# Optimization experiments

Measured on AMD Instinct MI355X. Metric: run time of the kernel, lower is better.

The kernel has to match this reference:

```python
import jax, jax.numpy as jnp
import numpy as np

H = 512
A = 16
L = 3
B = 256
T = 512


def layer_norm(x, g, b, eps=1e-5):
    mu = jnp.mean(x, axis=-1, keepdims=True)
    var = jnp.mean((x - mu) ** 2, axis=-1, keepdims=True)
    return (x - mu) * jax.lax.rsqrt(var + eps) * g + b


def setup_inputs() -> dict:
    key = jax.random.key(0)
    ks = jax.random.split(key, 16)
    s = 1.0 / np.sqrt(H)  # keep linear outputs O(1), mimicking orthogonal init scale
    return {
        "hidden": jnp.zeros((B, H), jnp.float32),
        "obs": jax.random.normal(ks[0], (B, T, H), jnp.float32),
        "dones": jax.random.bernoulli(ks[1], 0.01, (B, T)),
        "avail_actions": jnp.ones((B, T, A), jnp.float32),
        "in_w": jax.random.normal(ks[2], (L, H, H), jnp.float32) * s,
        "in_b": jnp.zeros((L, H), jnp.float32),
        "ln_g": jnp.ones((L, H), jnp.float32),
        "ln_b": jnp.zeros((L, H), jnp.float32),
        "gru_wih": jax.random.normal(ks[3], (3 * H, H), jnp.float32) * s,
        "gru_whh": jax.random.normal(ks[4], (3 * H, H), jnp.float32) * s,
        "gru_bih": jnp.zeros((3 * H,), jnp.float32),
        "gru_bhh": jnp.zeros((3 * H,), jnp.float32),
        "am1_w": jax.random.normal(ks[5], (H, H), jnp.float32) * s,
        "am1_b": jnp.zeros((H,), jnp.float32),
        "amln_g": jnp.ones((H,), jnp.float32),
        "amln_b": jnp.zeros((H,), jnp.float32),
        "am2_w": jax.random.normal(ks[6], (A, H), jnp.float32) * s * 0.01,
        "am2_b": jnp.zeros((A,), jnp.float32),
    }


def reference(hidden, obs, dones, avail_actions, in_w, in_b, ln_g, ln_b,
              gru_wih, gru_whh, gru_bih, gru_bhh,
              am1_w, am1_b, amln_g, amln_b, am2_w, am2_b):
    # --- pre-RNN MLP: Linear -> LayerNorm -> ReLU, x3 ---
    emb = obs  # [B,T,H]
    for l in range(L):
        emb = jax.nn.relu(layer_norm(emb @ in_w[l].T + in_b[l], ln_g[l], ln_b[l]))

    # --- GRU scan with reset masking (torch GRUCell math) ---
    def step(h, xt):
        x, r = xt  # x: [B,H], r: [B] bool
        h = jnp.where(r[:, None], 0.0, h)
        gi = x @ gru_wih.T + gru_bih  # [B,3H]
        gh = h @ gru_whh.T + gru_bhh
        i_r, i_z, i_n = jnp.split(gi, 3, axis=-1)
        h_r, h_z, h_n = jnp.split(gh, 3, axis=-1)
        rg = jax.nn.sigmoid(i_r + h_r)
        z = jax.nn.sigmoid(i_z + h_z)
        n = jnp.tanh(i_n + rg * h_n)
        h_new = (1.0 - z) * n + z * h
        return h_new, h_new

    h_final, outs = jax.lax.scan(
        step, hidden, (jnp.swapaxes(emb, 0, 1), dones.T))  # outs: [T,B,H]
    outs = jnp.swapaxes(outs, 0, 1)  # [B,T,H]

    # --- actor head ---
    am = jax.nn.relu(layer_norm(outs @ am1_w.T + am1_b, amln_g, amln_b))
    logits = am @ am2_w.T + am2_b  # [B,T,A]
    logits = logits - (1.0 - avail_actions) * 1e10
    return (h_final, logits)
```

## Files before the change

kernel.cpp:

```cpp
#include <hip/hip_runtime.h>

#define HD 512
#define AD 16
#define BD 256
#define TD 512

using short8  = __attribute__((ext_vector_type(8))) short;
using float4v = __attribute__((ext_vector_type(4))) float;
using ushort4v = __attribute__((ext_vector_type(4))) unsigned short;
typedef unsigned short u16;
typedef unsigned long long u64;

__device__ __forceinline__ u16 f2bf(float f) {
  union { float f; unsigned u; } v; v.f = f;
  unsigned r = v.u + 0x7fffu + ((v.u >> 16) & 1u);
  return (u16)(r >> 16);
}
__device__ __forceinline__ float bf2f(u16 u) {
  union { unsigned u; float f; } c; c.u = ((unsigned)u) << 16; return c.f;
}

__global__ __launch_bounds__(256) void cvt_bf16(const float* __restrict__ in,
                                                u16* __restrict__ out, int n) {
  int i = blockIdx.x * 256 + threadIdx.x;
  int stride = gridDim.x * 256;
  for (; i < n; i += stride) out[i] = f2bf(in[i]);
}

template <bool AF32>
__global__ __launch_bounds__(256) void gemm_ln_relu(
    const void* __restrict__ Ap, const u16* __restrict__ W,
    const float* __restrict__ bias, const float* __restrict__ gam,
    const float* __restrict__ bet, u16* __restrict__ Y) {
  const int r0 = blockIdx.x * 64;
  const int tid = threadIdx.x;
  const int wave = tid >> 6, lane = tid & 63;
  const int lq = lane >> 4, ln16 = lane & 15;

  __shared__ u16 As[64 * 40];
  __shared__ u16 Bs[512 * 40];
  __shared__ float partial[64][4][2];
  __shared__ float murs[64][2];

  float4v acc[4][8];
#pragma unroll
  for (int i = 0; i < 4; ++i)
#pragma unroll
    for (int j = 0; j < 8; ++j) acc[i][j] = (float4v){0.f, 0.f, 0.f, 0.f};

  for (int kk = 0; kk < 16; ++kk) {
    __syncthreads();
    if (AF32) {
      const float* Af = (const float*)Ap;
#pragma unroll
      for (int it = 0; it < 2; ++it) {
        int q = tid + it * 256;
        int row = q >> 3, ko = (q & 7) * 4;
        float4v v = *(const float4v*)(Af + (r0 + row) * 512 + kk * 32 + ko);
        ushort4v o;
        o[0] = f2bf(v[0]); o[1] = f2bf(v[1]); o[2] = f2bf(v[2]); o[3] = f2bf(v[3]);
        *(ushort4v*)(&As[row * 40 + ko]) = o;
      }
    } else {
      const u16* Ab = (const u16*)Ap;
      int row = tid >> 2, ko = (tid & 3) * 8;
      *(short8*)(&As[row * 40 + ko]) =
          *(const short8*)(Ab + (r0 + row) * 512 + kk * 32 + ko);
    }
#pragma unroll
    for (int it = 0; it < 8; ++it) {
      int q = tid + it * 256;
      int row = q >> 2, ko = (q & 3) * 8;
      *(short8*)(&Bs[row * 40 + ko]) =
          *(const short8*)(W + row * 512 + kk * 32 + ko);
    }
    __syncthreads();
    short8 afr[4];
#pragma unroll
    for (int mt = 0; mt < 4; ++mt)
      afr[mt] = *(const short8*)(&As[(mt * 16 + ln16) * 40 + lq * 8]);
#pragma unroll
    for (int nt = 0; nt < 8; ++nt) {
      short8 bfr = *(const short8*)(&Bs[(wave * 128 + nt * 16 + ln16) * 40 + lq * 8]);
#pragma unroll
      for (int mt = 0; mt < 4; ++mt)
        acc[mt][nt] = __builtin_amdgcn_mfma_f32_16x16x32_bf16(afr[mt], bfr, acc[mt][nt], 0, 0, 0);
    }
  }

  float gv[8], bv[8], av[8];
#pragma unroll
  for (int nt = 0; nt < 8; ++nt) {
    int c = wave * 128 + nt * 16 + ln16;
    gv[nt] = gam[c]; bv[nt] = bet[c]; av[nt] = bias[c];
  }
#pragma unroll
  for (int mt = 0; mt < 4; ++mt)
#pragma unroll
    for (int nt = 0; nt < 8; ++nt)
#pragma unroll
      for (int r = 0; r < 4; ++r) acc[mt][nt][r] += av[nt];

#pragma unroll
  for (int mt = 0; mt < 4; ++mt) {
#pragma unroll
    for (int r = 0; r < 4; ++r) {
      float s = 0.f, ss = 0.f;
#pragma unroll
      for (int nt = 0; nt < 8; ++nt) { float v = acc[mt][nt][r]; s += v; ss += v * v; }
#pragma unroll
      for (int off = 1; off < 16; off <<= 1) { s += __shfl_xor(s, off); ss += __shfl_xor(ss, off); }
      if (ln16 == 0) {
        int m = mt * 16 + lq * 4 + r;
        partial[m][wave][0] = s; partial[m][wave][1] = ss;
      }
    }
  }
  __syncthreads();
  if (tid < 64) {
    float s = partial[tid][0][0] + partial[tid][1][0] + partial[tid][2][0] + partial[tid][3][0];
    float ss = partial[tid][0][1] + partial[tid][1][1] + partial[tid][2][1] + partial[tid][3][1];
    float mu = s * (1.f / 512.f);
    float var = ss * (1.f / 512.f) - mu * mu;
    murs[tid][0] = mu;
    murs[tid][1] = rsqrtf(var + 1e-5f);
  }
  __syncthreads();
#pragma unroll
  for (int mt = 0; mt < 4; ++mt) {
#pragma unroll
    for (int r = 0; r < 4; ++r) {
      int m = mt * 16 + lq * 4 + r;
      float mu = murs[m][0], rs = murs[m][1];
#pragma unroll
      for (int nt = 0; nt < 8; ++nt) {
        int c = wave * 128 + nt * 16 + ln16;
        float v = (acc[mt][nt][r] - mu) * rs * gv[nt] + bv[nt];
        Y[(r0 + m) * 512 + c] = f2bf(fmaxf(v, 0.f));
      }
    }
  }
}

__global__ __launch_bounds__(256) void gru_scan(
    const u16* __restrict__ emb, const u16* __restrict__ wih,
    const u16* __restrict__ whh, const float* __restrict__ bih,
    const float* __restrict__ bhh, const float* __restrict__ hidden,
    const int* __restrict__ dones, float* __restrict__ outs,
    float* __restrict__ hfin, u64* __restrict__ hpk, int* __restrict__ cnt) {
  const int bg = blockIdx.x >> 5;
  const int cg = blockIdx.x & 31;
  const int c0 = cg * 16;
  const int b0 = bg * 32;
  const int tid = threadIdx.x;
  const int wave = tid >> 6, lane = tid & 63;
  const int lq = lane >> 4, ln16 = lane & 15;

  __shared__ u16 Wh[48 * 512];
  __shared__ float scr[2][2][3][16][18];

  for (int q = tid; q < 48 * 64; q += 256) {
    int rr = q >> 6, c = q & 63;
    int gate = rr >> 4, chl = rr & 15;
    int phys = c ^ (rr & 7);
    *(short8*)(&Wh[rr * 512 + phys * 8]) =
        *(const short8*)(whh + (gate * 512 + c0 + chl) * 512 + c * 8);
  }

  auto produce = [&](int tp, int mt) {
    int row = b0 + mt * 16 + ln16;
    const u16* ap = emb + (row * 512 + tp) * 512 + lq * 8;
    float4v acc[3];
#pragma unroll
    for (int g = 0; g < 3; ++g) acc[g] = (float4v){0.f, 0.f, 0.f, 0.f};
#pragma unroll
    for (int kk = 0; kk < 16; ++kk) {
      short8 af = *(const short8*)(ap + kk * 32);
#pragma unroll
      for (int g = 0; g < 3; ++g) {
        short8 bf = *(const short8*)(wih + (g * 512 + c0 + ln16) * 512 + lq * 8 + kk * 32);
        acc[g] = __builtin_amdgcn_mfma_f32_16x16x32_bf16(af, bf, acc[g], 0, 0, 0);
      }
    }
#pragma unroll
    for (int g = 0; g < 3; ++g)
#pragma unroll
      for (int r = 0; r < 4; ++r)
        scr[tp & 1][mt][g][lq * 4 + r][ln16] = acc[g][r];
  };

  if (wave >= 2) produce(0, wave - 2);
  __syncthreads();

  if (wave < 2) {
    const int mt = wave;
    const int rowA = b0 + mt * 16 + ln16;
    float bi[3], bhv[3];
#pragma unroll
    for (int g = 0; g < 3; ++g) {
      bi[g]  = bih[g * 512 + c0 + ln16];
      bhv[g] = bhh[g * 512 + c0 + ln16];
    }
    float hprev[4];
#pragma unroll
    for (int r = 0; r < 4; ++r)
      hprev[r] = hidden[(b0 + mt * 16 + lq * 4 + r) * 512 + c0 + ln16];

    int* mycnt = cnt + (bg * 2 + mt) * 512;

    for (int t = 0; t < TD; ++t) {
      bool dn = dones[rowA * 512 + t] != 0;
      int dn_i = dn ? 1 : 0;
      float giv[3][4];
#pragma unroll
      for (int g = 0; g < 3; ++g)
#pragma unroll
        for (int r = 0; r < 4; ++r) giv[g][r] = scr[t & 1][mt][g][lq * 4 + r][ln16];

      if (t > 0) {
        const int* cp = mycnt + (t - 1);
        int guard = 0;
        while (__hip_atomic_load(cp, __ATOMIC_RELAXED, __HIP_MEMORY_SCOPE_AGENT) < 32) {
          if (++guard > (1 << 18)) break;
        }
      }

      u64 av[32];
      if (t == 0) {
#pragma unroll
        for (int kk = 0; kk < 16; ++kk) {
          const float* hp = hidden + rowA * 512 + lq * 8 + kk * 32;
          float4v h0 = *(const float4v*)(hp);
          float4v h1 = *(const float4v*)(hp + 4);
          av[2 * kk] = (u64)f2bf(h0[0]) | ((u64)f2bf(h0[1]) << 16) |
                       ((u64)f2bf(h0[2]) << 32) | ((u64)f2bf(h0[3]) << 48);
          av[2 * kk + 1] = (u64)f2bf(h1[0]) | ((u64)f2bf(h1[1]) << 16) |
                           ((u64)f2bf(h1[2]) << 32) | ((u64)f2bf(h1[3]) << 48);
        }
      } else {
        const u64* hb = hpk + ((t - 1) & 1) * 32768 + rowA * 128 + lq * 2;
#pragma unroll
        for (int kk = 0; kk < 16; ++kk) {
          av[2 * kk]     = __hip_atomic_load(hb + kk * 8,     __ATOMIC_RELAXED, __HIP_MEMORY_SCOPE_AGENT);
          av[2 * kk + 1] = __hip_atomic_load(hb + kk * 8 + 1, __ATOMIC_RELAXED, __HIP_MEMORY_SCOPE_AGENT);
        }
      }
#pragma unroll
      for (int i = 0; i < 32; ++i) av[i] = dn ? 0ull : av[i];

      float4v agh[3];
#pragma unroll
      for (int g = 0; g < 3; ++g) agh[g] = (float4v){0.f, 0.f, 0.f, 0.f};
#pragma unroll
      for (int kk = 0; kk < 16; ++kk) {
        union { u64 q[2]; short8 v; } u;
        u.q[0] = av[2 * kk]; u.q[1] = av[2 * kk + 1];
#pragma unroll
        for (int g = 0; g < 3; ++g) {
          int rr = g * 16 + ln16;
          int phys = (lq + 4 * kk) ^ (rr & 7);
          short8 bf = *(const short8*)(&Wh[rr * 512 + phys * 8]);
          agh[g] = __builtin_amdgcn_mfma_f32_16x16x32_bf16(u.v, bf, agh[g], 0, 0, 0);
        }
      }

      float hv[4];
#pragma unroll
      for (int r = 0; r < 4; ++r) {
        int dnc = __shfl(dn_i, lq * 4 + r);
        float h = dnc ? 0.f : hprev[r];
        float ir  = giv[0][r] + bi[0];
        float iz  = giv[1][r] + bi[1];
        float inn = giv[2][r] + bi[2];
        float hr  = agh[0][r] + bhv[0];
        float hz  = agh[1][r] + bhv[1];
        float hn  = agh[2][r] + bhv[2];
        float rg = 1.f / (1.f + expf(-(ir + hr)));
        float z  = 1.f / (1.f + expf(-(iz + hz)));
        float nn = tanhf(inn + rg * hn);
        hv[r] = (1.f - z) * nn + z * h;
        hprev[r] = hv[r];
      }

#pragma unroll
      for (int r = 0; r < 4; ++r) {
        unsigned mybf = f2bf(hv[r]);
        unsigned o1 = (unsigned)__shfl((int)mybf, lane ^ 1);
        unsigned pk = (mybf & 0xffffu) | (o1 << 16);
        unsigned pk2 = (unsigned)__shfl((int)pk, lane ^ 2);
        int b = b0 + mt * 16 + lq * 4 + r;
        if ((ln16 & 3) == 0) {
          u64 pv = (u64)pk | ((u64)pk2 << 32);
          __hip_atomic_store(hpk + (t & 1) * 32768 + b * 128 + ((c0 + ln16) >> 2), pv,
                             __ATOMIC_RELAXED, __HIP_MEMORY_SCOPE_AGENT);
        }
        outs[(t * 256 + b) * 512 + c0 + ln16] = hv[r];
        if (t == TD - 1) hfin[b * 512 + c0 + ln16] = hv[r];
      }
      __builtin_amdgcn_s_waitcnt(0);
      if (lane == 0 && t < TD - 1)
        __hip_atomic_fetch_add(mycnt + t, 1, __ATOMIC_RELAXED, __HIP_MEMORY_SCOPE_AGENT);

      __syncthreads();
    }
  } else {
    const int mt = wave - 2;
    for (int t = 0; t < TD; ++t) {
      if (t + 1 < TD) produce(t + 1, mt);
      __syncthreads();
    }
  }
}

__global__ __launch_bounds__(256) void head_logits(
    const u16* __restrict__ am, const float* __restrict__ w2,
    const float* __restrict__ b2, const float* __restrict__ avail,
    float* __restrict__ out) {
  int r = blockIdx.x * 16 + (threadIdx.x >> 4);
  int a = threadIdx.x & 15;
  int t = r >> 8, b = r & 255;
  const u16* ar = am + r * 512;
  const float* wr = w2 + a * 512;
  float acc = 0.f;
  for (int k = 0; k < 512; k += 8) {
    short8 v = *(const short8*)(ar + k);
    float4v w0 = *(const float4v*)(wr + k);
    float4v w1 = *(const float4v*)(wr + k + 4);
    acc += bf2f((u16)v[0]) * w0[0] + bf2f((u16)v[1]) * w0[1] +
           bf2f((u16)v[2]) * w0[2] + bf2f((u16)v[3]) * w0[3] +
           bf2f((u16)v[4]) * w1[0] + bf2f((u16)v[5]) * w1[1] +
           bf2f((u16)v[6]) * w1[2] + bf2f((u16)v[7]) * w1[3];
  }
  int oi = (b * 512 + t) * 16 + a;
  float avv = avail[oi];
  out[oi] = acc + b2[a] - (1.f - avv) * 1e10f;
}

extern "C" void kernel_launch(void* const* d_in, const int* in_sizes, int n_in,
                              void* d_out, int out_size, void* d_ws, size_t ws_size,
                              hipStream_t stream) {
  (void)in_sizes; (void)n_in; (void)out_size; (void)ws_size;
  const float* hidden = (const float*)d_in[0];
  const float* obs    = (const float*)d_in[1];
  const int*   dones  = (const int*)d_in[2];
  const float* avail  = (const float*)d_in[3];
  const float* in_w   = (const float*)d_in[4];
  const float* in_b   = (const float*)d_in[5];
  const float* ln_g   = (const float*)d_in[6];
  const float* ln_b   = (const float*)d_in[7];
  const float* gwih   = (const float*)d_in[8];
  const float* gwhh   = (const float*)d_in[9];
  const float* gbih   = (const float*)d_in[10];
  const float* gbhh   = (const float*)d_in[11];
  const float* am1w   = (const float*)d_in[12];
  const float* am1b   = (const float*)d_in[13];
  const float* amg    = (const float*)d_in[14];
  const float* amb    = (const float*)d_in[15];
  const float* am2w   = (const float*)d_in[16];
  const float* am2b   = (const float*)d_in[17];

  char* ws = (char*)d_ws;
  u16*   embA  = (u16*)(ws);
  u16*   embB  = (u16*)(ws + 134217728);
  float* outs  = (float*)(ws + 268435456);
  u16*   w_in  = (u16*)(ws + 536870912);
  u16*   w_ih  = w_in + 786432;
  u16*   w_hh  = w_ih + 786432;
  u16*   w_a1  = w_hh + 786432;
  int*   cnt   = (int*)(ws + 536870912 + 5242880);
  u64*   hpk   = (u64*)(ws + 536870912 + 5242880 + 32768);

  hipMemsetAsync(cnt, 0, 32768, stream);
  cvt_bf16<<<1024, 256, 0, stream>>>(in_w, w_in, 786432);
  cvt_bf16<<<1024, 256, 0, stream>>>(gwih, w_ih, 786432);
  cvt_bf16<<<1024, 256, 0, stream>>>(gwhh, w_hh, 786432);
  cvt_bf16<<<512, 256, 0, stream>>>(am1w, w_a1, 262144);

  gemm_ln_relu<true ><<<2048, 256, 0, stream>>>(obs,  w_in,          in_b,        ln_g,        ln_b,        embA);
  gemm_ln_relu<false><<<2048, 256, 0, stream>>>(embA, w_in + 262144, in_b + 512,  ln_g + 512,  ln_b + 512,  embB);
  gemm_ln_relu<false><<<2048, 256, 0, stream>>>(embB, w_in + 524288, in_b + 1024, ln_g + 1024, ln_b + 1024, embA);

  gru_scan<<<256, 256, 0, stream>>>(embA, w_ih, w_hh, gbih, gbhh, hidden, dones,
                                    outs, (float*)d_out, hpk, cnt);

  gemm_ln_relu<true ><<<2048, 256, 0, stream>>>(outs, w_a1, am1b, amg, amb, embB);
  head_logits<<<8192, 256, 0, stream>>>(embB, am2w, am2b, avail, (float*)d_out + 131072);
}
```

Baseline: 4.751 ms.

## Keep GRU weights in registers, use fast sigmoid/tanh, and signal before output stores

The recurrent W_hh slice and the input W_ih slice now live in per-lane registers (48 short8 each) instead of LDS or repeated global reads, with launch bounds set to one block per CU. Gate activations use exp2/rcp hardware intrinsics instead of expf/tanhf. Done-masking now zeroes the h·W_hh products per row instead of masking the packed inputs. Each lane stores its bf16 h value directly rather than shuffle-packing into 64-bit words, and the readiness counter is bumped before the fp32 output stores so dependent blocks can start sooner. The intent is to shorten the serial per-step critical path, at the cost of very high register pressure, possible spills, and slightly less accurate transcendentals.

```diff
diff --git a/kernel.cpp b/kernel.cpp
--- a/kernel.cpp
+++ b/kernel.cpp
@@ -18,6 +18,13 @@
 }
 __device__ __forceinline__ float bf2f(u16 u) {
   union { unsigned u; float f; } c; c.u = ((unsigned)u) << 16; return c.f;
+}
+__device__ __forceinline__ float fsigm(float x) {
+  return __builtin_amdgcn_rcpf(1.f + __builtin_amdgcn_exp2f(-1.4426950408889634f * x));
+}
+__device__ __forceinline__ float ftanh(float x) {
+  float e = __builtin_amdgcn_exp2f(2.8853900817779268f * x);
+  return 1.f - 2.f * __builtin_amdgcn_rcpf(1.f + e);
 }
 
 __global__ __launch_bounds__(256) void cvt_bf16(const float* __restrict__ in,
@@ -142,7 +149,7 @@
   }
 }
 
-__global__ __launch_bounds__(256) void gru_scan(
+__global__ __launch_bounds__(256, 1) void gru_scan(
     const u16* __restrict__ emb, const u16* __restrict__ wih,
     const u16* __restrict__ whh, const float* __restrict__ bih,
     const float* __restrict__ bhh, const float* __restrict__ hidden,
@@ -156,45 +163,21 @@
   const int wave = tid >> 6, lane = tid & 63;
   const int lq = lane >> 4, ln16 = lane & 15;
 
-  __shared__ u16 Wh[48 * 512];
   __shared__ float scr[2][2][3][16][18];
-
-  for (int q = tid; q < 48 * 64; q += 256) {
-    int rr = q >> 6, c = q & 63;
-    int gate = rr >> 4, chl = rr & 15;
-    int phys = c ^ (rr & 7);
-    *(short8*)(&Wh[rr * 512 + phys * 8]) =
-        *(const short8*)(whh + (gate * 512 + c0 + chl) * 512 + c * 8);
-  }
-
-  auto produce = [&](int tp, int mt) {
-    int row = b0 + mt * 16 + ln16;
-    const u16* ap = emb + (row * 512 + tp) * 512 + lq * 8;
-    float4v acc[3];
-#pragma unroll
-    for (int g = 0; g < 3; ++g) acc[g] = (float4v){0.f, 0.f, 0.f, 0.f};
-#pragma unroll
-    for (int kk = 0; kk < 16; ++kk) {
-      short8 af = *(const short8*)(ap + kk * 32);
-#pragma unroll
-      for (int g = 0; g < 3; ++g) {
-        short8 bf = *(const short8*)(wih + (g * 512 + c0 + ln16) * 512 + lq * 8 + kk * 32);
-        acc[g] = __builtin_amdgcn_mfma_f32_16x16x32_bf16(af, bf, acc[g], 0, 0, 0);
-      }
-    }
-#pragma unroll
-    for (int g = 0; g < 3; ++g)
-#pragma unroll
-      for (int r = 0; r < 4; ++r)
-        scr[tp & 1][mt][g][lq * 4 + r][ln16] = acc[g][r];
-  };
-
-  if (wave >= 2) produce(0, wave - 2);
-  __syncthreads();
+  u16* hpk16 = (u16*)hpk;
 
   if (wave < 2) {
     const int mt = wave;
     const int rowA = b0 + mt * 16 + ln16;
+
+    short8 wr_[48];
+#pragma unroll
+    for (int g = 0; g < 3; ++g)
+#pragma unroll
+      for (int kk = 0; kk < 16; ++kk)
+        wr_[g * 16 + kk] =
+            *(const short8*)(whh + (g * 512 + c0 + ln16) * 512 + kk * 32 + lq * 8);
+
     float bi[3], bhv[3];
 #pragma unroll
     for (int g = 0; g < 3; ++g) {
@@ -208,9 +191,13 @@
 
     int* mycnt = cnt + (bg * 2 + mt) * 512;
 
+    __syncthreads();
+
     for (int t = 0; t < TD; ++t) {
-      bool dn = dones[rowA * 512 + t] != 0;
-      int dn_i = dn ? 1 : 0;
+      int dnr[4];
+#pragma unroll
+      for (int r = 0; r < 4; ++r)
+        dnr[r] = dones[(b0 + mt * 16 + lq * 4 + r) * 512 + t];
       float giv[3][4];
 #pragma unroll
       for (int g = 0; g < 3; ++g)
@@ -238,15 +225,13 @@
                            ((u64)f2bf(h1[2]) << 32) | ((u64)f2bf(h1[3]) << 48);
         }
       } else {
-        const u64* hb = hpk + ((t - 1) & 1) * 32768 + rowA * 128 + lq * 2;
+        u64* hb = hpk + ((t - 1) & 1) * 32768 + rowA * 128 + lq * 2;
 #pragma unroll
         for (int kk = 0; kk < 16; ++kk) {
           av[2 * kk]     = __hip_atomic_load(hb + kk * 8,     __ATOMIC_RELAXED, __HIP_MEMORY_SCOPE_AGENT);
           av[2 * kk + 1] = __hip_atomic_load(hb + kk * 8 + 1, __ATOMIC_RELAXED, __HIP_MEMORY_SCOPE_AGENT);
         }
       }
-#pragma unroll
-      for (int i = 0; i < 32; ++i) av[i] = dn ? 0ull : av[i];
 
       float4v agh[3];
 #pragma unroll
@@ -256,57 +241,79 @@
         union { u64 q[2]; short8 v; } u;
         u.q[0] = av[2 * kk]; u.q[1] = av[2 * kk + 1];
 #pragma unroll
-        for (int g = 0; g < 3; ++g) {
-          int rr = g * 16 + ln16;
-          int phys = (lq + 4 * kk) ^ (rr & 7);
-          short8 bf = *(const short8*)(&Wh[rr * 512 + phys * 8]);
-          agh[g] = __builtin_amdgcn_mfma_f32_16x16x32_bf16(u.v, bf, agh[g], 0, 0, 0);
-        }
+        for (int g = 0; g < 3; ++g)
+          agh[g] = __builtin_amdgcn_mfma_f32_16x16x32_bf16(u.v, wr_[g * 16 + kk], agh[g], 0, 0, 0);
       }
 
       float hv[4];
 #pragma unroll
       for (int r = 0; r < 4; ++r) {
-        int dnc = __shfl(dn_i, lq * 4 + r);
-        float h = dnc ? 0.f : hprev[r];
-        float ir  = giv[0][r] + bi[0];
-        float iz  = giv[1][r] + bi[1];
-        float inn = giv[2][r] + bi[2];
-        float hr  = agh[0][r] + bhv[0];
-        float hz  = agh[1][r] + bhv[1];
-        float hn  = agh[2][r] + bhv[2];
-        float rg = 1.f / (1.f + expf(-(ir + hr)));
-        float z  = 1.f / (1.f + expf(-(iz + hz)));
-        float nn = tanhf(inn + rg * hn);
+        bool d = dnr[r] != 0;
+        float h  = d ? 0.f : hprev[r];
+        float g0 = d ? 0.f : agh[0][r];
+        float g1 = d ? 0.f : agh[1][r];
+        float g2 = d ? 0.f : agh[2][r];
+        float rg = fsigm(giv[0][r] + bi[0] + g0 + bhv[0]);
+        float z  = fsigm(giv[1][r] + bi[1] + g1 + bhv[1]);
+        float nn = ftanh(giv[2][r] + bi[2] + rg * (g2 + bhv[2]));
         hv[r] = (1.f - z) * nn + z * h;
         hprev[r] = hv[r];
       }
 
 #pragma unroll
       for (int r = 0; r < 4; ++r) {
-        unsigned mybf = f2bf(hv[r]);
-        unsigned o1 = (unsigned)__shfl((int)mybf, lane ^ 1);
-        unsigned pk = (mybf & 0xffffu) | (o1 << 16);
-        unsigned pk2 = (unsigned)__shfl((int)pk, lane ^ 2);
         int b = b0 + mt * 16 + lq * 4 + r;
-        if ((ln16 & 3) == 0) {
-          u64 pv = (u64)pk | ((u64)pk2 << 32);
-          __hip_atomic_store(hpk + (t & 1) * 32768 + b * 128 + ((c0 + ln16) >> 2), pv,
-                             __ATOMIC_RELAXED, __HIP_MEMORY_SCOPE_AGENT);
-        }
+        __hip_atomic_store(hpk16 + (t & 1) * 131072 + b * 512 + c0 + ln16,
+                           f2bf(hv[r]), __ATOMIC_RELAXED, __HIP_MEMORY_SCOPE_AGENT);
+      }
+      asm volatile("s_waitcnt vmcnt(0)" ::: "memory");
+      if (lane == 0 && t < TD - 1)
+        __hip_atomic_fetch_add(mycnt + t, 1, __ATOMIC_RELAXED, __HIP_MEMORY_SCOPE_AGENT);
+
+#pragma unroll
+      for (int r = 0; r < 4; ++r) {
+        int b = b0 + mt * 16 + lq * 4 + r;
         outs[(t * 256 + b) * 512 + c0 + ln16] = hv[r];
         if (t == TD - 1) hfin[b * 512 + c0 + ln16] = hv[r];
       }
-      __builtin_amdgcn_s_waitcnt(0);
-      if (lane == 0 && t < TD - 1)
-        __hip_atomic_fetch_add(mycnt + t, 1, __ATOMIC_RELAXED, __HIP_MEMORY_SCOPE_AGENT);
-
       __syncthreads();
     }
   } else {
     const int mt = wave - 2;
+
+    short8 wf[48];
+#pragma unroll
+    for (int g = 0; g < 3; ++g)
+#pragma unroll
+      for (int kk = 0; kk < 16; ++kk)
+        wf[g * 16 + kk] =
+            *(const short8*)(wih + (g * 512 + c0 + ln16) * 512 + kk * 32 + lq * 8);
+
+    const int row = b0 + mt * 16 + ln16;
+    auto produce = [&](int tp) {
+      const u16* ap = emb + (row * 512 + tp) * 512 + lq * 8;
+      float4v acc[3];
+#pragma unroll
+      for (int g = 0; g < 3; ++g) acc[g] = (float4v){0.f, 0.f, 0.f, 0.f};
+#pragma unroll
+      for (int kk = 0; kk < 16; ++kk) {
+        short8 af = *(const short8*)(ap + kk * 32);
+#pragma unroll
+        for (int g = 0; g < 3; ++g)
+          acc[g] = __builtin_amdgcn_mfma_f32_16x16x32_bf16(af, wf[g * 16 + kk], acc[g], 0, 0, 0);
+      }
+#pragma unroll
+      for (int g = 0; g < 3; ++g)
+#pragma unroll
+        for (int r = 0; r < 4; ++r)
+          scr[tp & 1][mt][g][lq * 4 + r][ln16] = acc[g][r];
+    };
+
+    produce(0);
+    __syncthreads();
+
     for (int t = 0; t < TD; ++t) {
-      if (t + 1 < TD) produce(t + 1, mt);
+      if (t + 1 < TD) produce(t + 1);
       __syncthreads();
     }
   }
```

After: 4.644 ms. 2.3% less time.
